# Performance work log

Measured on AMD Instinct MI355X. Metric: run time of the kernel, lower is better.

The kernel has to match this reference:

```python
import jax, jax.numpy as jnp
import numpy as np
from jax import lax

N_BOXES = 6000
IOU_THR = 0.5
CONF_THR = 0.6


def setup_inputs() -> dict:
    key = jax.random.key(0)
    k1, k2, k3 = jax.random.split(key, 3)
    # valid xyxy boxes: top-left in [0,1000), width/height in [1,101)
    xy = jax.random.uniform(k1, (N_BOXES, 2), dtype=jnp.float32) * 1000.0
    wh = jax.random.uniform(k2, (N_BOXES, 2), dtype=jnp.float32) * 100.0 + 1.0
    boxes = jnp.concatenate([xy, xy + wh], axis=-1)  # [N,4] x1,y1,x2,y2
    scores = jax.random.uniform(k3, (N_BOXES,), dtype=jnp.float32)
    return {"boxes": boxes, "scores": scores}


def _pairwise_iou(b):
    # b: [N,4] xyxy. Returns [N,N] IoU, coordinates handled separately to
    # avoid materializing [N,N,2] intermediates.
    x1, y1, x2, y2 = b[:, 0], b[:, 1], b[:, 2], b[:, 3]
    area = (x2 - x1) * (y2 - y1)  # [N]
    iw = jnp.clip(jnp.minimum(x2[:, None], x2[None, :]) - jnp.maximum(x1[:, None], x1[None, :]), 0.0)
    ih = jnp.clip(jnp.minimum(y2[:, None], y2[None, :]) - jnp.maximum(y1[:, None], y1[None, :]), 0.0)
    inter = iw * ih  # [N,N]
    return inter / (area[:, None] + area[None, :] - inter)


def reference(boxes, scores):
    """torchvision-style NMS (suppress IoU > 0.5) then confidence filter (>= 0.6).
    Returns masked scores [N]: score where the box survives both stages, else 0.
    (Fixed-shape mask form of the original index outputs, for jit compatibility.)
    """
    n = scores.shape[0]
    order = jnp.argsort(-scores)  # descending by confidence
    iou = _pairwise_iou(boxes[order])  # [N,N] in sorted order
    idx = jnp.arange(n)

    def body(suppressed, i):
        keep_i = jnp.logical_not(suppressed[i])
        # a kept box suppresses all lower-scoring boxes with IoU > threshold
        supp_new = keep_i & (iou[i] > IOU_THR) & (idx > i)
        return suppressed | supp_new, keep_i

    _, keep_sorted = lax.scan(body, jnp.zeros((n,), dtype=bool), idx)
    keep = jnp.zeros((n,), dtype=bool).at[order].set(keep_sorted)
    final = keep & (scores >= CONF_THR)
    return jnp.where(final, scores, 0.0)
```

## Files before the change

kernel.cpp:

```cpp
#include <hip/hip_runtime.h>
#include <stdint.h>

#define N_BOXES 6000
#define NT 94
#define NTP 96
#define NROWS (NTP * 64)
#define CAP 16
#define IOU_THR 0.5f
#define CONF_THR 0.6f

typedef unsigned long long u64;
typedef unsigned int u32;
typedef unsigned short u16;

#define BAR() asm volatile("s_waitcnt lgkmcnt(0)\n\ts_barrier" ::: "memory")

__device__ __forceinline__ u64 rdlane64(u64 v, int l) {
    unsigned lo = (unsigned)__builtin_amdgcn_readlane((int)(unsigned)v, l);
    unsigned hi = (unsigned)__builtin_amdgcn_readlane((int)(unsigned)(v >> 32), l);
    return ((u64)hi << 32) | lo;
}

__global__ void __launch_bounds__(1024) k_sort(const float* __restrict__ scores,
                                               const float4* __restrict__ boxes,
                                               int* __restrict__ sidx,
                                               float4* __restrict__ sboxes,
                                               u32* __restrict__ lists_w,
                                               int* __restrict__ cnt) {
    __shared__ u64 kt[N_BOXES];
    __shared__ int part[1024];
    const int tid = threadIdx.x;
    const int gtid = blockIdx.x * 1024 + tid;
    for (int j = gtid; j < NROWS * CAP / 2; j += NT * 1024) lists_w[j] = 0xFFFFFFFFu;
    for (int j = gtid; j < NROWS; j += NT * 1024) cnt[j] = 0;

    for (int j = tid; j < N_BOXES; j += 1024) {
        unsigned inv = ~__float_as_uint(scores[j]);
        kt[j] = ((u64)inv << 32) | (unsigned)j;
    }
    __syncthreads();
    const int il = tid & 63;
    const int i = blockIdx.x * 64 + il;
    const int j0 = (tid >> 6) * 375;
    u64 mykey = (i < N_BOXES) ? kt[i] : 0ull;
    int cntr = 0;
#pragma unroll 5
    for (int jj = 0; jj < 375; ++jj)
        cntr += (kt[j0 + jj] < mykey) ? 1 : 0;
    part[tid] = cntr;
    __syncthreads();
    if (tid < 64 && i < N_BOXES) {
        int r = 0;
#pragma unroll
        for (int s = 0; s < 16; ++s) r += part[il + 64 * s];
        sidx[r] = i;
        sboxes[r] = boxes[i];
    }
}

__global__ void k_mask(const float4* __restrict__ sboxes,
                       u16* __restrict__ lists, int* __restrict__ cnt,
                       u64* __restrict__ diagw) {
    int ct = blockIdx.x, rt = blockIdx.y;
    if (ct < rt) return;
    int lane = threadIdx.x;
    __shared__ float4 rb[64];
    int row0 = rt * 64;
    int rows = min(64, N_BOXES - row0);
    if (lane < rows) rb[lane] = sboxes[row0 + lane];
    __syncthreads();
    int j = ct * 64 + lane;
    bool jvalid = (j < N_BOXES);
    float4 cb = make_float4(0.f, 0.f, 1.f, 1.f);
    if (jvalid) cb = sboxes[j];
    float carea = (cb.z - cb.x) * (cb.w - cb.y);
    bool isdiag = (ct == rt);
    for (int i = 0; i < rows; ++i) {
        float4 rbx = rb[i];
        float rarea = (rbx.z - rbx.x) * (rbx.w - rbx.y);
        float iw = fmaxf(fminf(rbx.z, cb.z) - fmaxf(rbx.x, cb.x), 0.f);
        float ih = fmaxf(fminf(rbx.w, cb.w) - fmaxf(rbx.y, cb.y), 0.f);
        float inter = iw * ih;
        float iou = inter / ((rarea + carea) - inter);
        int row = row0 + i;
        bool pred = jvalid && (j > row) && (iou > IOU_THR);
        if (isdiag) {
            u64 bal = __ballot(pred);
            if (lane == (i & 63)) diagw[row] = bal;
        } else if (pred) {
            int slot = atomicAdd(&cnt[row], 1);
            if (slot < CAP) lists[row * CAP + slot] = (u16)j;
        }
    }
}

__global__ void __launch_bounds__(256) k_scan(const u16* __restrict__ lists,
                                              const u64* __restrict__ diagw,
                                              const int* __restrict__ sidx,
                                              const float* __restrict__ scores,
                                              float* __restrict__ out) {
    __shared__ u64 removed[NTP];
    __shared__ u64 kwbuf[NTP];
    const int tid   = threadIdx.x;
    const int lane  = tid & 63;
    const int row_l = tid >> 2;
    const int sg    = (tid & 3) * 4;
    if (tid < NTP) removed[tid] = 0;

    u64 L0, L1, L2, D0, D1, D2;
    L0 = *(const u64*)&lists[(0 * 64 + row_l) * CAP + sg];
    L1 = *(const u64*)&lists[(1 * 64 + row_l) * CAP + sg];
    L2 = *(const u64*)&lists[(2 * 64 + row_l) * CAP + sg];
    D0 = diagw[0 * 64 + lane];
    D1 = diagw[1 * 64 + lane];
    D2 = diagw[2 * 64 + lane];
    __syncthreads();

#define STEP(T, LUSE, DUSE)                                                    \
    {                                                                          \
        const u64 nz = __ballot(DUSE != 0ull);        \
        const int row0 = (T) * 64;                                             \
        const int rem = N_BOXES - row0;                                        \
        const u64 valid = (rem >= 64) ? ~0ull                                  \
                        : ((rem <= 0) ? 0ull : ((1ull << rem) - 1ull));        \
        u64 c = valid & ~removed[(T)];                                         \
        u64 kw = 0;                                                            \
        while (c) {                                                            \
            u64 blockers = c & nz;                                             \
            if (!blockers) { kw |= c; break; }             \
            int g = (int)__builtin_ctzll(blockers);                            \
            u64 below = c & ((1ull << g) - 1ull);         \
            kw |= below | (1ull << g);                                         \
            u64 df = rdlane64(DUSE, g);                     \
            c &= ~(df | below | (1ull << g));                                  \
        }                                                                      \
        if (tid == 0) kwbuf[(T)] = kw;                                         \
        if (((kw >> row_l) & 1ull) && LUSE != ~0ull) {                         \
            u16 e0 = (u16)(LUSE), e1 = (u16)(LUSE >> 16),                      \
                e2 = (u16)(LUSE >> 32), e3 = (u16)(LUSE >> 48);                \
            if (e0 != 0xFFFFu) atomicOr(&removed[e0 >> 6], 1ull << (e0 & 63)); \
            if (e1 != 0xFFFFu) atomicOr(&removed[e1 >> 6], 1ull << (e1 & 63)); \
            if (e2 != 0xFFFFu) atomicOr(&removed[e2 >> 6], 1ull << (e2 & 63)); \
            if (e3 != 0xFFFFu) atomicOr(&removed[e3 >> 6], 1ull << (e3 & 63)); \
        }                                                                      \
        const int tn = ((T) + 3 < NTP) ? ((T) + 3) : ((T) + 3 - NTP);          \
        LUSE = *(const u64*)&lists[(tn * 64 + row_l) * CAP + sg];              \
        DUSE = diagw[tn * 64 + lane];                                          \
        BAR();                                                                 \
    }

    for (int t = 0; t < NTP; t += 3) {
        STEP(t,     L0, D0)
        STEP(t + 1, L1, D1)
        STEP(t + 2, L2, D2)
    }
#undef STEP

    for (int p = tid; p < N_BOXES; p += 256) {
        int orig = sidx[p];
        float s = scores[orig];
        bool k = (kwbuf[p >> 6] >> (p & 63)) & 1ull;
        out[orig] = (k && (s >= CONF_THR)) ? s : 0.0f;
    }
}

extern "C" void kernel_launch(void* const* d_in, const int* in_sizes, int n_in,
                              void* d_out, int out_size, void* d_ws, size_t ws_size,
                              hipStream_t stream) {
    const float* boxes  = (const float*)d_in[0];
    const float* scores = (const float*)d_in[1];
    float* out = (float*)d_out;

    char* ws = (char*)d_ws;
    u16*    lists  = (u16*)(ws);
    int*    cnt    = (int*)(ws + 196608);
    u64*    diagw  = (u64*)(ws + 221184);
    int*    sidx   = (int*)(ws + 270336);
    float4* sboxes = (float4*)(ws + 294336);

    k_sort<<<dim3(NT), dim3(1024), 0, stream>>>(scores, (const float4*)boxes, sidx,
                                                sboxes, (u32*)lists, cnt);
    k_mask<<<dim3(NT, NT), dim3(64), 0, stream>>>((const float4*)sboxes, lists, cnt, diagw);
    k_scan<<<dim3(1), dim3(256), 0, stream>>>(lists, diagw, sidx, scores, out);
}
```

Before: 132.7 us.

## Run NMS scan in a single wavefront without barriers; split output into own kernel

The serial scan kernel now runs as one 64-lane wavefront, with each lane owning a whole row's 16-entry suppression list, so the per-tile workgroup barrier is removed. Keep bitmasks go to global memory, and a separate 24-block kernel scatters the masked scores. This targets barrier and cross-wave sync latency on the serial critical path. In exchange, each lane issues more LDS atomics per step, it relies on in-wave ordering of LDS atomics for correctness, and there is an extra kernel launch.

Result: no change. 134.9 us (+1.6%).

```diff
diff --git a/kernel.cpp b/kernel.cpp
--- a/kernel.cpp
+++ b/kernel.cpp
@@ -12,8 +12,6 @@
 typedef unsigned long long u64;
 typedef unsigned int u32;
 typedef unsigned short u16;
-
-#define BAR() asm volatile("s_waitcnt lgkmcnt(0)\n\ts_barrier" ::: "memory")
 
 __device__ __forceinline__ u64 rdlane64(u64 v, int l) {
     unsigned lo = (unsigned)__builtin_amdgcn_readlane((int)(unsigned)v, l);
@@ -94,72 +92,79 @@
     }
 }
 
-__global__ void __launch_bounds__(256) k_scan(const u16* __restrict__ lists,
-                                              const u64* __restrict__ diagw,
-                                              const int* __restrict__ sidx,
-                                              const float* __restrict__ scores,
-                                              float* __restrict__ out) {
+__global__ void __launch_bounds__(64) k_scan(const u16* __restrict__ lists,
+                                             const u64* __restrict__ diagw,
+                                             u64* __restrict__ keep) {
     __shared__ u64 removed[NTP];
-    __shared__ u64 kwbuf[NTP];
-    const int tid   = threadIdx.x;
-    const int lane  = tid & 63;
-    const int row_l = tid >> 2;
-    const int sg    = (tid & 3) * 4;
-    if (tid < NTP) removed[tid] = 0;
+    const int lane = threadIdx.x;
+    removed[lane] = 0;
+    if (lane < NTP - 64) removed[64 + lane] = 0;
 
-    u64 L0, L1, L2, D0, D1, D2;
-    L0 = *(const u64*)&lists[(0 * 64 + row_l) * CAP + sg];
-    L1 = *(const u64*)&lists[(1 * 64 + row_l) * CAP + sg];
-    L2 = *(const u64*)&lists[(2 * 64 + row_l) * CAP + sg];
-    D0 = diagw[0 * 64 + lane];
-    D1 = diagw[1 * 64 + lane];
-    D2 = diagw[2 * 64 + lane];
-    __syncthreads();
+    u64 A0[3], A1[3], A2[3], A3[3], D[3];
+#pragma unroll
+    for (int b = 0; b < 3; ++b) {
+        const u64* lp = (const u64*)&lists[(b * 64 + lane) * CAP];
+        A0[b] = lp[0]; A1[b] = lp[1]; A2[b] = lp[2]; A3[b] = lp[3];
+        D[b] = diagw[b * 64 + lane];
+    }
 
-#define STEP(T, LUSE, DUSE)                                                    \
-    {                                                                          \
-        const u64 nz = __ballot(DUSE != 0ull);        \
-        const int row0 = (T) * 64;                                             \
-        const int rem = N_BOXES - row0;                                        \
-        const u64 valid = (rem >= 64) ? ~0ull                                  \
-                        : ((rem <= 0) ? 0ull : ((1ull << rem) - 1ull));        \
-        u64 c = valid & ~removed[(T)];                                         \
-        u64 kw = 0;                                                            \
-        while (c) {                                                            \
-            u64 blockers = c & nz;                                             \
-            if (!blockers) { kw |= c; break; }             \
-            int g = (int)__builtin_ctzll(blockers);                            \
-            u64 below = c & ((1ull << g) - 1ull);         \
-            kw |= below | (1ull << g);                                         \
-            u64 df = rdlane64(DUSE, g);                     \
-            c &= ~(df | below | (1ull << g));                                  \
-        }                                                                      \
-        if (tid == 0) kwbuf[(T)] = kw;                                         \
-        if (((kw >> row_l) & 1ull) && LUSE != ~0ull) {                         \
-            u16 e0 = (u16)(LUSE), e1 = (u16)(LUSE >> 16),                      \
-                e2 = (u16)(LUSE >> 32), e3 = (u16)(LUSE >> 48);                \
-            if (e0 != 0xFFFFu) atomicOr(&removed[e0 >> 6], 1ull << (e0 & 63)); \
-            if (e1 != 0xFFFFu) atomicOr(&removed[e1 >> 6], 1ull << (e1 & 63)); \
-            if (e2 != 0xFFFFu) atomicOr(&removed[e2 >> 6], 1ull << (e2 & 63)); \
-            if (e3 != 0xFFFFu) atomicOr(&removed[e3 >> 6], 1ull << (e3 & 63)); \
-        }                                                                      \
-        const int tn = ((T) + 3 < NTP) ? ((T) + 3) : ((T) + 3 - NTP);          \
-        LUSE = *(const u64*)&lists[(tn * 64 + row_l) * CAP + sg];              \
-        DUSE = diagw[tn * 64 + lane];                                          \
-        BAR();                                                                 \
+#define SCAT(W)                                                                 \
+    if (W != ~0ull) {                                                           \
+        u16 e0 = (u16)(W), e1 = (u16)(W >> 16),                                 \
+            e2 = (u16)(W >> 32), e3 = (u16)(W >> 48);                           \
+        if (e0 != 0xFFFFu) atomicOr(&removed[e0 >> 6], 1ull << (e0 & 63));      \
+        if (e1 != 0xFFFFu) atomicOr(&removed[e1 >> 6], 1ull << (e1 & 63));      \
+        if (e2 != 0xFFFFu) atomicOr(&removed[e2 >> 6], 1ull << (e2 & 63));      \
+        if (e3 != 0xFFFFu) atomicOr(&removed[e3 >> 6], 1ull << (e3 & 63));      \
+    }
+
+#define STEP(T, B)                                                              \
+    {                                                                           \
+        const u64 d = D[B];                                                     \
+        const u64 nz = __ballot(d != 0ull);            \
+        const int rem = N_BOXES - (T) * 64;                                     \
+        const u64 valid = (rem >= 64) ? ~0ull                                   \
+                        : ((rem <= 0) ? 0ull : ((1ull << rem) - 1ull));         \
+        u64 c = valid & ~removed[(T)];           \
+        u64 kw = 0;                                                             \
+        while (c) {                                                             \
+            u64 blockers = c & nz;                                              \
+            if (!blockers) { kw |= c; break; }              \
+            int g = (int)__builtin_ctzll(blockers);                             \
+            u64 below = c & ((1ull << g) - 1ull);                               \
+            kw |= below | (1ull << g);                                          \
+            u64 df = rdlane64(d, g);                         \
+            c &= ~(df | below | (1ull << g));                                   \
+        }                                                                       \
+        if (lane == 0) keep[(T)] = kw;                     \
+        if ((kw >> lane) & 1ull) {                                              \
+            u64 w0 = A0[B], w1 = A1[B], w2 = A2[B], w3 = A3[B];                 \
+            SCAT(w0) SCAT(w1) SCAT(w2) SCAT(w3)                                 \
+        }                                                                       \
+        const int tn = ((T) + 3 < NTP) ? ((T) + 3) : ((T) + 3 - NTP);           \
+        const u64* lp = (const u64*)&lists[(tn * 64 + lane) * CAP];             \
+        A0[B] = lp[0]; A1[B] = lp[1]; A2[B] = lp[2]; A3[B] = lp[3];             \
+        D[B] = diagw[tn * 64 + lane];                                           \
     }
 
     for (int t = 0; t < NTP; t += 3) {
-        STEP(t,     L0, D0)
-        STEP(t + 1, L1, D1)
-        STEP(t + 2, L2, D2)
+        STEP(t,     0)
+        STEP(t + 1, 1)
+        STEP(t + 2, 2)
     }
 #undef STEP
+#undef SCAT
+}
 
-    for (int p = tid; p < N_BOXES; p += 256) {
+__global__ void __launch_bounds__(256) k_out(const int* __restrict__ sidx,
+                                             const float* __restrict__ scores,
+                                             const u64* __restrict__ keep,
+                                             float* __restrict__ out) {
+    int p = blockIdx.x * 256 + threadIdx.x;
+    if (p < N_BOXES) {
         int orig = sidx[p];
         float s = scores[orig];
-        bool k = (kwbuf[p >> 6] >> (p & 63)) & 1ull;
+        bool k = (keep[p >> 6] >> (p & 63)) & 1ull;
         out[orig] = (k && (s >= CONF_THR)) ? s : 0.0f;
     }
 }
@@ -177,9 +182,11 @@
     u64*    diagw  = (u64*)(ws + 221184);
     int*    sidx   = (int*)(ws + 270336);
     float4* sboxes = (float4*)(ws + 294336);
+    u64*    keep   = (u64*)(ws + 390336);
 
     k_sort<<<dim3(NT), dim3(1024), 0, stream>>>(scores, (const float4*)boxes, sidx,
                                                 sboxes, (u32*)lists, cnt);
     k_mask<<<dim3(NT, NT), dim3(64), 0, stream>>>((const float4*)sboxes, lists, cnt, diagw);
-    k_scan<<<dim3(1), dim3(256), 0, stream>>>(lists, diagw, sidx, scores, out);
+    k_scan<<<dim3(1), dim3(64), 0, stream>>>(lists, diagw, keep);
+    k_out <<<dim3(24), dim3(256), 0, stream>>>(sidx, scores, keep, out);
 }
```
